# Kernel tuning notes

Hardware: AMD Instinct MI355X
Metric: run time of the kernel (lower is better)

The kernel has to match this reference:

```python
import jax, jax.numpy as jnp
import numpy as np

N_TOK = 4096      # total packed tokens
C = 256           # channels
H = 8             # num_heads
B = 8             # number of packed sequences
NEG = -10000.0    # additive mask value used by the torch module (not -inf)


def setup_inputs() -> dict:
    key = jax.random.key(0)
    ks = jax.random.split(key, 8)
    qkv = jax.random.normal(ks[0], (N_TOK, C), jnp.float32)
    q_pos = jax.random.normal(ks[1], (N_TOK, C), jnp.float32)
    # cu_seqlens: sorted prefix boundaries, 0 ... N_TOK (B segments)
    interior = jnp.sort(jax.random.randint(ks[2], (B - 1,), 1, N_TOK))
    cu_seqlens = jnp.concatenate([jnp.zeros((1,), jnp.int32),
                                  interior.astype(jnp.int32),
                                  jnp.full((1,), N_TOK, jnp.int32)])
    # xavier-uniform-ish scale for linear weights (stored as [in, out])
    def xavier(k, fan_in, fan_out):
        lim = np.sqrt(6.0 / (fan_in + fan_out)).astype(np.float32)
        return jax.random.uniform(k, (fan_in, fan_out), jnp.float32, -lim, lim)
    Wq = xavier(ks[3], C, C)
    Wkv = xavier(ks[4], C, 2 * C)
    Wproj = xavier(ks[5], C, C)
    bproj = jnp.zeros((C,), jnp.float32)
    return {"qkv": qkv, "q_pos": q_pos, "cu_seqlens": cu_seqlens,
            "max_seqlen": N_TOK, "Wq": Wq, "Wkv": Wkv,
            "Wproj": Wproj, "bproj": bproj}


def reference(qkv, q_pos, cu_seqlens, max_seqlen, Wq, Wkv, Wproj, bproj):
    N, Cdim = qkv.shape
    hd = Cdim // H
    scale = hd ** -0.5

    q = (qkv + q_pos) @ Wq                 # [N, C]
    kv = qkv @ Wkv                         # [N, 2C]
    k, v = kv[:, :Cdim], kv[:, Cdim:]

    # upcast_attention=True -> float32 attention (inputs already fp32)
    q = q.astype(jnp.float32).reshape(N, H, hd)
    k = k.astype(jnp.float32).reshape(N, H, hd)
    v = v.astype(jnp.float32).reshape(N, H, hd)

    # block-diagonal additive mask: segment id per token via searchsorted
    seg = jnp.searchsorted(cu_seqlens[1:], jnp.arange(N), side='right')
    bias = jnp.where(seg[:, None] == seg[None, :], 0.0, NEG)  # [N, N]

    scores = jnp.einsum('nhd,mhd->hnm', q, k) * scale + bias[None]  # [H,N,N]
    attn = jax.nn.softmax(scores, axis=-1)
    feat = jnp.einsum('hnm,mhd->nhd', attn, v).reshape(N, Cdim)
    feat = feat.astype(qkv.dtype)
    return feat @ Wproj + bproj
```

## Files before the change

### kernel.cpp

```cpp
#include <hip/hip_runtime.h>
#include <hip/hip_bf16.h>
#include <math.h>

#define NTOK 4096
#define CDIM 256
#define NH   8
#define HD   32
#define SCALE 0.17677669529663687f

typedef __attribute__((ext_vector_type(8))) short bf16x8;
typedef __attribute__((ext_vector_type(4))) short short4v;
typedef __attribute__((ext_vector_type(4))) float f32x4;

__device__ inline short f2b(float f) {
  union { __hip_bfloat16 h; short s; } u;
  u.h = __float2bfloat16(f);
  return u.s;
}
__device__ inline short4v pack4(f32x4 v) {
  short4v o; o[0] = f2b(v[0]); o[1] = f2b(v[1]); o[2] = f2b(v[2]); o[3] = f2b(v[3]);
  return o;
}

__global__ __launch_bounds__(256) void prep_kernel(
    const float* __restrict__ qkv, const float* __restrict__ qpos,
    const float* __restrict__ Wq, const float* __restrict__ Wkv,
    const float* __restrict__ Wp,
    short* __restrict__ Xq, short* __restrict__ X,
    short* __restrict__ WT, short* __restrict__ WpT)
{
  const int b = blockIdx.x, t = threadIdx.x;
  if (b < 1024) {
    const int i4 = (b * 256 + t) * 4;
    float4 a = *(const float4*)(qkv + i4);
    float4 p = *(const float4*)(qpos + i4);
    short4v xo, qo;
    xo[0] = f2b(a.x); xo[1] = f2b(a.y); xo[2] = f2b(a.z); xo[3] = f2b(a.w);
    qo[0] = f2b(a.x + p.x); qo[1] = f2b(a.y + p.y); qo[2] = f2b(a.z + p.z); qo[3] = f2b(a.w + p.w);
    *(short4v*)(X + i4)  = xo;
    *(short4v*)(Xq + i4) = qo;
  } else {
    const int gid = (b - 1024) * 256 + t;
    const int c  = gid & 1023;
    const int k4 = (gid >> 10) * 4;
    short4v o;
    if (c < 768) {
      #pragma unroll
      for (int j = 0; j < 4; ++j) {
        int k = k4 + j;
        float v = (c < 256) ? Wq[(size_t)k * 256 + c] * SCALE
                            : Wkv[(size_t)k * 512 + (c - 256)];
        o[j] = f2b(v);
      }
      *(short4v*)(WT + (size_t)c * 256 + k4) = o;
    } else {
      const int cc = c - 768;
      #pragma unroll
      for (int j = 0; j < 4; ++j) o[j] = f2b(Wp[(size_t)(k4 + j) * 256 + cc]);
      *(short4v*)(WpT + (size_t)cc * 256 + k4) = o;
    }
  }
}

__global__ __launch_bounds__(256) void gemm_qkv(
    const short* __restrict__ Xq, const short* __restrict__ X,
    const short* __restrict__ WT,
    short* __restrict__ qb, short* __restrict__ khp, short* __restrict__ vblk)
{
  __shared__ short Al[64][40];
  __shared__ short Wl[64][40];
  const int bx = blockIdx.x;
  const int n0 = blockIdx.y * 64;
  const int c0 = bx * 64;
  const int tid = threadIdx.x;
  const int w = tid >> 6, l = tid & 63, lg = l >> 4, lr = l & 15;
  const int wc = w & 1, wn = w >> 1;
  const short* A = (bx < 4) ? Xq : X;

  f32x4 acc[2][2];
  #pragma unroll
  for (int i = 0; i < 2; ++i)
    #pragma unroll
    for (int j = 0; j < 2; ++j) acc[i][j] = (f32x4){0.f, 0.f, 0.f, 0.f};

  for (int kt = 0; kt < 256; kt += 32) {
    __syncthreads();
    {
      int row = tid >> 2, seg = tid & 3;
      *(bf16x8*)&Al[row][seg * 8] = *(const bf16x8*)(A  + (size_t)(n0 + row) * 256 + kt + seg * 8);
      *(bf16x8*)&Wl[row][seg * 8] = *(const bf16x8*)(WT + (size_t)(c0 + row) * 256 + kt + seg * 8);
    }
    __syncthreads();
    bf16x8 wf[2], xf[2];
    #pragma unroll
    for (int ci = 0; ci < 2; ++ci) wf[ci] = *(bf16x8*)&Wl[wc * 32 + ci * 16 + lr][lg * 8];
    #pragma unroll
    for (int ni = 0; ni < 2; ++ni) xf[ni] = *(bf16x8*)&Al[wn * 32 + ni * 16 + lr][lg * 8];
    if (bx < 8) {
      #pragma unroll
      for (int ci = 0; ci < 2; ++ci)
        #pragma unroll
        for (int ni = 0; ni < 2; ++ni)
          acc[ci][ni] = __builtin_amdgcn_mfma_f32_16x16x32_bf16(wf[ci], xf[ni], acc[ci][ni], 0, 0, 0);
    } else {
      #pragma unroll
      for (int ci = 0; ci < 2; ++ci)
        #pragma unroll
        for (int ni = 0; ni < 2; ++ni)
          acc[ci][ni] = __builtin_amdgcn_mfma_f32_16x16x32_bf16(xf[ni], wf[ci], acc[ci][ni], 0, 0, 0);
    }
  }

  if (bx < 4) {
    const int cl0 = bx * 64;
    #pragma unroll
    for (int ci = 0; ci < 2; ++ci)
      #pragma unroll
      for (int ni = 0; ni < 2; ++ni) {
        int c = cl0 + wc * 32 + ci * 16 + lg * 4;
        int n = n0 + wn * 32 + ni * 16 + lr;
        *(short4v*)(qb + (size_t)n * 256 + c) = pack4(acc[ci][ni]);
      }
  } else if (bx < 8) {
    const int cl0 = (bx - 4) * 64;
    #pragma unroll
    for (int ci = 0; ci < 2; ++ci)
      #pragma unroll
      for (int ni = 0; ni < 2; ++ni) {
        int c = cl0 + wc * 32 + ci * 16 + lg * 4;
        int n = n0 + wn * 32 + ni * 16 + lr;
        int hh = c >> 5, d = c & 31;
        int tt = n >> 5, k = n & 31;
        int s = ((k >> 2) & 1) * 16 + (k >> 3) * 4 + (k & 3);
        *(short4v*)(khp + (((size_t)hh * 128 + tt) * 32 + s) * 32 + d) = pack4(acc[ci][ni]);
      }
  } else {
    const int cv0 = (bx - 8) * 64;
    #pragma unroll
    for (int ci = 0; ci < 2; ++ci)
      #pragma unroll
      for (int ni = 0; ni < 2; ++ni) {
        int c = cv0 + wc * 32 + ci * 16 + lr;
        int n = n0 + wn * 32 + ni * 16 + lg * 4;
        int hh = c >> 5, d = c & 31;
        int tt = n >> 5, k = n & 31;
        *(short4v*)(vblk + (((size_t)hh * 128 + tt) * 32 + d) * 32 + k) = pack4(acc[ci][ni]);
      }
  }
}

__global__ __launch_bounds__(256) void attn6(
    const short* __restrict__ qb, const short* __restrict__ khp,
    const short* __restrict__ vblk, const int* __restrict__ cu,
    short* __restrict__ featb)
{
  __shared__ float red[4][64][9];
  const int tid = threadIdx.x;
  const int w = tid >> 6, l = tid & 63, lg = l >> 4, lr = l & 15;
  const int bid = blockIdx.x;
  const int lid = ((bid & 7) << 8) | (bid >> 3);
  const int h = lid & 7, t = lid >> 3;
  const int n0 = t * 16;

  int cs[9];
  #pragma unroll
  for (int i = 0; i < 9; ++i) cs[i] = cu[i];

  const int qn = n0 + lr;
  int sg = 0, sg0 = 0, sgL = 0;
  #pragma unroll
  for (int j = 1; j <= 8; ++j) {
    sg  += (cs[j] <= qn);
    sg0 += (cs[j] <= n0);
    sgL += (cs[j] <= n0 + 15);
  }
  const int kbegL = cs[sg], kendL = cs[sg + 1];
  const int lo = cs[sg0] & ~31;
  const int hi = cs[sgL + 1];
  const int t0 = lo >> 5;
  const int nT = (hi - lo + 31) >> 5;
  const int qT = (nT + 3) >> 2;
  const int it0 = w * qT;
  const int it1 = (it0 + qT < nT) ? (it0 + qT) : nT;

  const bf16x8 qf = *(const bf16x8*)(qb + (size_t)qn * 256 + h * 32 + lg * 8);
  const short* kL = khp  + (size_t)h * 131072 + lr * 32 + lg * 8;
  const short* vL = vblk + (size_t)h * 131072 + lr * 32 + lg * 8;

  f32x4 acc0 = {0.f, 0.f, 0.f, 0.f}, acc1 = {0.f, 0.f, 0.f, 0.f};
  float Lp = 0.f;
  const f32x4 z4 = {0.f, 0.f, 0.f, 0.f};

  if (it0 < it1) {
    const short* kp = kL + (size_t)(t0 + it0) * 1024;
    const short* vp = vL + (size_t)(t0 + it0) * 1024;
    bf16x8 ka = *(const bf16x8*)(kp);
    bf16x8 kc = *(const bf16x8*)(kp + 512);
    bf16x8 va = *(const bf16x8*)(vp);
    bf16x8 vb = *(const bf16x8*)(vp + 512);
    for (int it = it0; it < it1; ++it) {
      const int itn = (it + 1 < it1) ? (it + 1) : it;
      const short* kpn = kL + (size_t)(t0 + itn) * 1024;
      const short* vpn = vL + (size_t)(t0 + itn) * 1024;
      bf16x8 kna = *(const bf16x8*)(kpn);
      bf16x8 knc = *(const bf16x8*)(kpn + 512);
      bf16x8 vna = *(const bf16x8*)(vpn);
      bf16x8 vnb = *(const bf16x8*)(vpn + 512);

      f32x4 s0 = __builtin_amdgcn_mfma_f32_16x16x32_bf16(ka, qf, z4, 0, 0, 0);
      f32x4 s1 = __builtin_amdgcn_mfma_f32_16x16x32_bf16(kc, qf, z4, 0, 0, 0);

      const int kgb = (t0 + it) * 32 + lg * 8;
      bf16x8 pf;
      #pragma unroll
      for (int r = 0; r < 4; ++r) {
        int k0 = kgb + r;
        bool ok0 = (k0 >= kbegL) & (k0 < kendL);
        float p0 = ok0 ? __expf(s0[r]) : 0.f;
        int k1 = kgb + 4 + r;
        bool ok1 = (k1 >= kbegL) & (k1 < kendL);
        float p1 = ok1 ? __expf(s1[r]) : 0.f;
        Lp += p0 + p1;
        pf[r]     = f2b(p0);
        pf[4 + r] = f2b(p1);
      }
      acc0 = __builtin_amdgcn_mfma_f32_16x16x32_bf16(pf, va, acc0, 0, 0, 0);
      acc1 = __builtin_amdgcn_mfma_f32_16x16x32_bf16(pf, vb, acc1, 0, 0, 0);

      ka = kna; kc = knc; va = vna; vb = vnb;
    }
  }

  #pragma unroll
  for (int r = 0; r < 4; ++r) { red[w][l][r] = acc0[r]; red[w][l][4 + r] = acc1[r]; }
  red[w][l][8] = Lp;
  __syncthreads();
  if (w == 0) {
    float a0[4] = {0.f, 0.f, 0.f, 0.f}, a1[4] = {0.f, 0.f, 0.f, 0.f}, Ls = 0.f;
    #pragma unroll
    for (int wv = 0; wv < 4; ++wv) {
      #pragma unroll
      for (int r = 0; r < 4; ++r) { a0[r] += red[wv][l][r]; a1[r] += red[wv][l][4 + r]; }
      Ls += red[wv][l][8];
    }
    Ls += __shfl_xor(Ls, 16);
    Ls += __shfl_xor(Ls, 32);
    float inv = 1.f / Ls;
    #pragma unroll
    for (int r = 0; r < 4; ++r) {
      float iq = __shfl(inv, lg * 4 + r);
      int n = n0 + lg * 4 + r;
      featb[(size_t)n * 256 + h * 32 + lr]      = f2b(a0[r] * iq);
      featb[(size_t)n * 256 + h * 32 + 16 + lr] = f2b(a1[r] * iq);
    }
  }
}

__global__ __launch_bounds__(256) void gemm_out(
    const short* __restrict__ Fb, const short* __restrict__ WpT,
    const float* __restrict__ bias, float* __restrict__ out)
{
  __shared__ short Al[64][40];
  __shared__ short Wl[64][40];
  const int c0 = blockIdx.x * 64;
  const int n0 = blockIdx.y * 64;
  const int tid = threadIdx.x;
  const int w = tid >> 6, l = tid & 63, lg = l >> 4, lr = l & 15;
  const int wc = w & 1, wn = w >> 1;

  f32x4 acc[2][2];
  #pragma unroll
  for (int i = 0; i < 2; ++i)
    #pragma unroll
    for (int j = 0; j < 2; ++j) acc[i][j] = (f32x4){0.f, 0.f, 0.f, 0.f};

  for (int kt = 0; kt < 256; kt += 32) {
    __syncthreads();
    {
      int row = tid >> 2, seg = tid & 3;
      *(bf16x8*)&Al[row][seg * 8] = *(const bf16x8*)(Fb  + (size_t)(n0 + row) * 256 + kt + seg * 8);
      *(bf16x8*)&Wl[row][seg * 8] = *(const bf16x8*)(WpT + (size_t)(c0 + row) * 256 + kt + seg * 8);
    }
    __syncthreads();
    bf16x8 wf[2], xf[2];
    #pragma unroll
    for (int ci = 0; ci < 2; ++ci) wf[ci] = *(bf16x8*)&Wl[wc * 32 + ci * 16 + lr][lg * 8];
    #pragma unroll
    for (int ni = 0; ni < 2; ++ni) xf[ni] = *(bf16x8*)&Al[wn * 32 + ni * 16 + lr][lg * 8];
    #pragma unroll
    for (int ci = 0; ci < 2; ++ci)
      #pragma unroll
      for (int ni = 0; ni < 2; ++ni)
        acc[ci][ni] = __builtin_amdgcn_mfma_f32_16x16x32_bf16(wf[ci], xf[ni], acc[ci][ni], 0, 0, 0);
  }

  #pragma unroll
  for (int ci = 0; ci < 2; ++ci)
    #pragma unroll
    for (int ni = 0; ni < 2; ++ni) {
      int c = c0 + wc * 32 + ci * 16 + lg * 4;
      int n = n0 + wn * 32 + ni * 16 + lr;
      f32x4 bv = *(const f32x4*)(bias + c);
      f32x4 o = acc[ci][ni] + bv;
      *(f32x4*)(out + (size_t)n * 256 + c) = o;
    }
}

extern "C" void kernel_launch(void* const* d_in, const int* in_sizes, int n_in,
                              void* d_out, int out_size, void* d_ws, size_t ws_size,
                              hipStream_t stream) {
  (void)in_sizes; (void)n_in; (void)out_size; (void)ws_size;
  const float* qkv   = (const float*)d_in[0];
  const float* q_pos = (const float*)d_in[1];
  const int*   cu    = (const int*)d_in[2];
  const float* Wq    = (const float*)d_in[4];
  const float* Wkv   = (const float*)d_in[5];
  const float* Wproj = (const float*)d_in[6];
  const float* bproj = (const float*)d_in[7];
  float* out = (float*)d_out;

  const size_t M = (size_t)NTOK * CDIM;
  short* S    = (short*)d_ws;
  short* Xq   = S;
  short* X    = S + M;
  short* qb   = S + 2 * M;
  short* khp  = S + 3 * M;
  short* vblk = S + 4 * M;
  short* Fb   = S + 5 * M;
  short* WT   = S + 6 * M;
  short* WpT  = WT + 768 * 256;

  prep_kernel<<<1280, 256, 0, stream>>>(qkv, q_pos, Wq, Wkv, Wproj, Xq, X, WT, WpT);
  gemm_qkv<<<dim3(12, 64), 256, 0, stream>>>(Xq, X, WT, qb, khp, vblk);
  attn6<<<2048, 256, 0, stream>>>(qb, khp, vblk, cu, Fb);
  gemm_out<<<dim3(4, 64), 256, 0, stream>>>(Fb, WpT, bproj, out);
}
```

Before: 44.90 us.

## Process 32 queries per attention block to reuse K/V tiles, skip masking on interior tiles

The attention kernel now handles two 16-query groups per block, so each K and V fragment loaded from memory feeds twice as many MFMAs, and the grid is halved. It also adds a fast path that skips the per-element segment mask checks when the whole block lies in one sequence and the key tile is fully inside it. The cost is more registers per thread, a larger shared reduction buffer, and fewer blocks to spread across compute units.

```diff
diff --git a/kernel.cpp b/kernel.cpp
--- a/kernel.cpp
+++ b/kernel.cpp
@@ -149,46 +149,52 @@
   }
 }
 
-__global__ __launch_bounds__(256) void attn6(
+__global__ __launch_bounds__(256) void attn7(
     const short* __restrict__ qb, const short* __restrict__ khp,
     const short* __restrict__ vblk, const int* __restrict__ cu,
     short* __restrict__ featb)
 {
-  __shared__ float red[4][64][9];
+  __shared__ float red[4][64][18];
   const int tid = threadIdx.x;
   const int w = tid >> 6, l = tid & 63, lg = l >> 4, lr = l & 15;
   const int bid = blockIdx.x;
-  const int lid = ((bid & 7) << 8) | (bid >> 3);
-  const int h = lid & 7, t = lid >> 3;
-  const int n0 = t * 16;
+  const int lid = ((bid & 7) << 7) | (bid >> 3);
+  const int h = lid & 7, t32 = lid >> 3;
+  const int n0 = t32 * 32;
 
   int cs[9];
   #pragma unroll
   for (int i = 0; i < 9; ++i) cs[i] = cu[i];
 
-  const int qn = n0 + lr;
-  int sg = 0, sg0 = 0, sgL = 0;
+  const int qn0 = n0 + lr, qn1 = n0 + 16 + lr;
+  int g0 = 0, g1 = 0, sg0 = 0, sgL = 0;
   #pragma unroll
   for (int j = 1; j <= 8; ++j) {
-    sg  += (cs[j] <= qn);
+    g0  += (cs[j] <= qn0);
+    g1  += (cs[j] <= qn1);
     sg0 += (cs[j] <= n0);
-    sgL += (cs[j] <= n0 + 15);
-  }
-  const int kbegL = cs[sg], kendL = cs[sg + 1];
-  const int lo = cs[sg0] & ~31;
-  const int hi = cs[sgL + 1];
+    sgL += (cs[j] <= n0 + 31);
+  }
+  const int kbeg0 = cs[g0], kend0 = cs[g0 + 1];
+  const int kbeg1 = cs[g1], kend1 = cs[g1 + 1];
+  const bool oneSeg = (sg0 == sgL);
+  const int kbB = cs[sg0], keB = cs[sgL + 1];
+  const int lo = kbB & ~31;
+  const int hi = keB;
   const int t0 = lo >> 5;
   const int nT = (hi - lo + 31) >> 5;
   const int qT = (nT + 3) >> 2;
   const int it0 = w * qT;
   const int it1 = (it0 + qT < nT) ? (it0 + qT) : nT;
 
-  const bf16x8 qf = *(const bf16x8*)(qb + (size_t)qn * 256 + h * 32 + lg * 8);
+  const bf16x8 qf0 = *(const bf16x8*)(qb + (size_t)qn0 * 256 + h * 32 + lg * 8);
+  const bf16x8 qf1 = *(const bf16x8*)(qb + (size_t)qn1 * 256 + h * 32 + lg * 8);
   const short* kL = khp  + (size_t)h * 131072 + lr * 32 + lg * 8;
   const short* vL = vblk + (size_t)h * 131072 + lr * 32 + lg * 8;
 
-  f32x4 acc0 = {0.f, 0.f, 0.f, 0.f}, acc1 = {0.f, 0.f, 0.f, 0.f};
-  float Lp = 0.f;
+  f32x4 acc00 = {0.f,0.f,0.f,0.f}, acc01 = {0.f,0.f,0.f,0.f};
+  f32x4 acc10 = {0.f,0.f,0.f,0.f}, acc11 = {0.f,0.f,0.f,0.f};
+  float Lp0 = 0.f, Lp1 = 0.f;
   const f32x4 z4 = {0.f, 0.f, 0.f, 0.f};
 
   if (it0 < it1) {
@@ -207,51 +213,86 @@
       bf16x8 vna = *(const bf16x8*)(vpn);
       bf16x8 vnb = *(const bf16x8*)(vpn + 512);
 
-      f32x4 s0 = __builtin_amdgcn_mfma_f32_16x16x32_bf16(ka, qf, z4, 0, 0, 0);
-      f32x4 s1 = __builtin_amdgcn_mfma_f32_16x16x32_bf16(kc, qf, z4, 0, 0, 0);
-
-      const int kgb = (t0 + it) * 32 + lg * 8;
-      bf16x8 pf;
-      #pragma unroll
-      for (int r = 0; r < 4; ++r) {
-        int k0 = kgb + r;
-        bool ok0 = (k0 >= kbegL) & (k0 < kendL);
-        float p0 = ok0 ? __expf(s0[r]) : 0.f;
-        int k1 = kgb + 4 + r;
-        bool ok1 = (k1 >= kbegL) & (k1 < kendL);
-        float p1 = ok1 ? __expf(s1[r]) : 0.f;
-        Lp += p0 + p1;
-        pf[r]     = f2b(p0);
-        pf[4 + r] = f2b(p1);
-      }
-      acc0 = __builtin_amdgcn_mfma_f32_16x16x32_bf16(pf, va, acc0, 0, 0, 0);
-      acc1 = __builtin_amdgcn_mfma_f32_16x16x32_bf16(pf, vb, acc1, 0, 0, 0);
+      f32x4 s00 = __builtin_amdgcn_mfma_f32_16x16x32_bf16(ka, qf0, z4, 0, 0, 0);
+      f32x4 s01 = __builtin_amdgcn_mfma_f32_16x16x32_bf16(kc, qf0, z4, 0, 0, 0);
+      f32x4 s10 = __builtin_amdgcn_mfma_f32_16x16x32_bf16(ka, qf1, z4, 0, 0, 0);
+      f32x4 s11 = __builtin_amdgcn_mfma_f32_16x16x32_bf16(kc, qf1, z4, 0, 0, 0);
+
+      const int kt0 = (t0 + it) * 32;
+      bf16x8 pf0, pf1;
+      if (oneSeg & (kt0 >= kbB) & (kt0 + 32 <= keB)) {
+        #pragma unroll
+        for (int r = 0; r < 4; ++r) {
+          float p00 = __expf(s00[r]), p01 = __expf(s01[r]);
+          float p10 = __expf(s10[r]), p11 = __expf(s11[r]);
+          Lp0 += p00 + p01; Lp1 += p10 + p11;
+          pf0[r] = f2b(p00); pf0[4 + r] = f2b(p01);
+          pf1[r] = f2b(p10); pf1[4 + r] = f2b(p11);
+        }
+      } else {
+        const int kgb = kt0 + lg * 8;
+        #pragma unroll
+        for (int r = 0; r < 4; ++r) {
+          int k0 = kgb + r, k1 = kgb + 4 + r;
+          bool a00 = (k0 >= kbeg0) & (k0 < kend0);
+          bool a01 = (k1 >= kbeg0) & (k1 < kend0);
+          bool a10 = (k0 >= kbeg1) & (k0 < kend1);
+          bool a11 = (k1 >= kbeg1) & (k1 < kend1);
+          float p00 = a00 ? __expf(s00[r]) : 0.f;
+          float p01 = a01 ? __expf(s01[r]) : 0.f;
+          float p10 = a10 ? __expf(s10[r]) : 0.f;
+          float p11 = a11 ? __expf(s11[r]) : 0.f;
+          Lp0 += p00 + p01; Lp1 += p10 + p11;
+          pf0[r] = f2b(p00); pf0[4 + r] = f2b(p01);
+          pf1[r] = f2b(p10); pf1[4 + r] = f2b(p11);
+        }
+      }
+      acc00 = __builtin_amdgcn_mfma_f32_16x16x32_bf16(pf0, va, acc00, 0, 0, 0);
+      acc01 = __builtin_amdgcn_mfma_f32_16x16x32_bf16(pf0, vb, acc01, 0, 0, 0);
+      acc10 = __builtin_amdgcn_mfma_f32_16x16x32_bf16(pf1, va, acc10, 0, 0, 0);
+      acc11 = __builtin_amdgcn_mfma_f32_16x16x32_bf16(pf1, vb, acc11, 0, 0, 0);
 
       ka = kna; kc = knc; va = vna; vb = vnb;
     }
   }
 
   #pragma unroll
-  for (int r = 0; r < 4; ++r) { red[w][l][r] = acc0[r]; red[w][l][4 + r] = acc1[r]; }
-  red[w][l][8] = Lp;
+  for (int r = 0; r < 4; ++r) {
+    red[w][l][r]      = acc00[r];
+    red[w][l][4 + r]  = acc01[r];
+    red[w][l][8 + r]  = acc10[r];
+    red[w][l][12 + r] = acc11[r];
+  }
+  red[w][l][16] = Lp0;
+  red[w][l][17] = Lp1;
   __syncthreads();
   if (w == 0) {
-    float a0[4] = {0.f, 0.f, 0.f, 0.f}, a1[4] = {0.f, 0.f, 0.f, 0.f}, Ls = 0.f;
+    float a00[4] = {0,0,0,0}, a01[4] = {0,0,0,0};
+    float a10[4] = {0,0,0,0}, a11[4] = {0,0,0,0};
+    float Ls0 = 0.f, Ls1 = 0.f;
     #pragma unroll
     for (int wv = 0; wv < 4; ++wv) {
       #pragma unroll
-      for (int r = 0; r < 4; ++r) { a0[r] += red[wv][l][r]; a1[r] += red[wv][l][4 + r]; }
-      Ls += red[wv][l][8];
-    }
-    Ls += __shfl_xor(Ls, 16);
-    Ls += __shfl_xor(Ls, 32);
-    float inv = 1.f / Ls;
+      for (int r = 0; r < 4; ++r) {
+        a00[r] += red[wv][l][r];      a01[r] += red[wv][l][4 + r];
+        a10[r] += red[wv][l][8 + r];  a11[r] += red[wv][l][12 + r];
+      }
+      Ls0 += red[wv][l][16];
+      Ls1 += red[wv][l][17];
+    }
+    Ls0 += __shfl_xor(Ls0, 16); Ls0 += __shfl_xor(Ls0, 32);
+    Ls1 += __shfl_xor(Ls1, 16); Ls1 += __shfl_xor(Ls1, 32);
+    float inv0 = 1.f / Ls0, inv1 = 1.f / Ls1;
     #pragma unroll
     for (int r = 0; r < 4; ++r) {
-      float iq = __shfl(inv, lg * 4 + r);
-      int n = n0 + lg * 4 + r;
-      featb[(size_t)n * 256 + h * 32 + lr]      = f2b(a0[r] * iq);
-      featb[(size_t)n * 256 + h * 32 + 16 + lr] = f2b(a1[r] * iq);
+      float i0 = __shfl(inv0, lg * 4 + r);
+      float i1 = __shfl(inv1, lg * 4 + r);
+      int na = n0 + lg * 4 + r;
+      int nb = n0 + 16 + lg * 4 + r;
+      featb[(size_t)na * 256 + h * 32 + lr]      = f2b(a00[r] * i0);
+      featb[(size_t)na * 256 + h * 32 + 16 + lr] = f2b(a01[r] * i0);
+      featb[(size_t)nb * 256 + h * 32 + lr]      = f2b(a10[r] * i1);
+      featb[(size_t)nb * 256 + h * 32 + 16 + lr] = f2b(a11[r] * i1);
     }
   }
 }
@@ -332,6 +373,6 @@
 
   prep_kernel<<<1280, 256, 0, stream>>>(qkv, q_pos, Wq, Wkv, Wproj, Xq, X, WT, WpT);
   gemm_qkv<<<dim3(12, 64), 256, 0, stream>>>(Xq, X, WT, qb, khp, vblk);
-  attn6<<<2048, 256, 0, stream>>>(qb, khp, vblk, cu, Fb);
+  attn7<<<1024, 256, 0, stream>>>(qb, khp, vblk, cu, Fb);
   gemm_out<<<dim3(4, 64), 256, 0, stream>>>(Fb, WpT, bproj, out);
 }
```

Measured after the change: 39.48 us. -12.1%, faster.
